# Kernel optimization log

Measured on AMD Instinct MI355X. Metric: run time of the kernel, lower is better.

Reference implementation:

```python
import jax, jax.numpy as jnp
import numpy as np

B, S, D = 4, 2048, 1024
D_K, D_V = 1024, 1024


def setup_inputs() -> dict:
    key = jax.random.key(0)
    ks = jax.random.split(key, 9)
    s = 1.0 / np.sqrt(D)
    return {
        "q_in": jax.random.normal(ks[0], (B, S, D), jnp.float32),
        "k_in": jax.random.normal(ks[1], (B, S, D), jnp.float32),
        "v_in": jax.random.normal(ks[2], (B, S, D), jnp.float32),
        "Wq": jax.random.normal(ks[3], (D, D_K), jnp.float32) * s,
        "bq": jnp.zeros((D_K,), jnp.float32),
        "Wk": jax.random.normal(ks[4], (D, D_K), jnp.float32) * s,
        "bk": jnp.zeros((D_K,), jnp.float32),
        "Wv": jax.random.normal(ks[5], (D, D_V), jnp.float32) * s,
        "bv": jnp.zeros((D_V,), jnp.float32),
    }


def reference(q_in, k_in, v_in, Wq, bq, Wk, bk, Wv, bv):
    q = jnp.einsum("bsd,dk->bsk", q_in, Wq) + bq  # [B,S,d_k]
    k = jnp.einsum("bsd,dk->bsk", k_in, Wk) + bk  # [B,S,d_k]
    v = jnp.einsum("bsd,dv->bsv", v_in, Wv) + bv  # [B,S,d_v]
    scores = jnp.einsum("bqk,bsk->bqs", q, k) / jnp.sqrt(jnp.float32(D_K))
    attn = jax.nn.softmax(scores, axis=-1)  # [B,S,S]
    return jnp.einsum("bqs,bsv->bqv", attn, v)
```

## Files before the change

kernel.cpp:

```cpp
#include <hip/hip_runtime.h>
#include <stdint.h>

#define B_  4
#define S_  2048
#define D_  1024
#define DK_ 1024
#define DV_ 1024

typedef __attribute__((ext_vector_type(8)))  short short8;
typedef __attribute__((ext_vector_type(16))) float floatx16;

#define ASYNC16(gsrc, ldst)                                                        \
  __builtin_amdgcn_global_load_lds(                                                \
      (const __attribute__((address_space(1))) unsigned int*)(gsrc),               \
      (__attribute__((address_space(3))) unsigned int*)(ldst), 16, 0, 0)

__device__ __forceinline__ unsigned short f2bf(float f) {
  union { float f; uint32_t u; } v; v.f = f;
  uint32_t r = v.u + 0x7fffu + ((v.u >> 16) & 1u);
  return (unsigned short)(r >> 16);
}

__global__ __launch_bounds__(256) void cvt_f32_bf16(const float* __restrict__ in,
                                                    unsigned short* __restrict__ out, int n4) {
  int i = blockIdx.x * blockDim.x + threadIdx.x;
  if (i >= n4) return;
  float4 v = ((const float4*)in)[i];
  ushort4 o;
  o.x = f2bf(v.x); o.y = f2bf(v.y); o.z = f2bf(v.z); o.w = f2bf(v.w);
  ((ushort4*)out)[i] = o;
}

__global__ __launch_bounds__(256) void transpose_f32_bf16(const float* __restrict__ in,
                                                          unsigned short* __restrict__ out,
                                                          int rows, int cols) {
  __shared__ float tile[32][33];
  int bx = blockIdx.x * 32, by = blockIdx.y * 32;
  int tx = threadIdx.x & 31, ty = threadIdx.x >> 5;
  for (int r = ty; r < 32; r += 8)
    tile[r][tx] = in[(long)(by + r) * cols + bx + tx];
  __syncthreads();
  for (int r = ty; r < 32; r += 8)
    out[(long)(bx + r) * rows + by + tx] = f2bf(tile[tx][r]);
}

__global__ __launch_bounds__(256) void transpose_bf16_batched(const unsigned short* __restrict__ in,
                                                              unsigned short* __restrict__ out,
                                                              int rows, int cols) {
  in  += (long)blockIdx.z * rows * cols;
  out += (long)blockIdx.z * rows * cols;
  __shared__ unsigned short tile[32][33];
  int bx = blockIdx.x * 32, by = blockIdx.y * 32;
  int tx = threadIdx.x & 31, ty = threadIdx.x >> 5;
  for (int r = ty; r < 32; r += 8)
    tile[r][tx] = in[(long)(by + r) * cols + bx + tx];
  __syncthreads();
  for (int r = ty; r < 32; r += 8)
    out[(long)(bx + r) * rows + by + tx] = tile[tx][r];
}

__device__ __forceinline__ void storeC(float* p, float v)          { *p = v; }
__device__ __forceinline__ void storeC(unsigned short* p, float v) { *p = f2bf(v); }

template <typename OutT, int NOUT>
__global__ __launch_bounds__(256)
void gemm_bt32(const unsigned short* __restrict__ A0, const unsigned short* __restrict__ A1,
               const unsigned short* __restrict__ A2, const unsigned short* __restrict__ Bm,
               OutT* __restrict__ C0, OutT* __restrict__ C1, OutT* __restrict__ C2,
               const float* __restrict__ b0, const float* __restrict__ b1,
               const float* __restrict__ b2,
               int N, int K, long sA, long sB, long sC, float scale) {
  __shared__ __align__(16) unsigned short As[2][128 * 32];
  __shared__ __align__(16) unsigned short Bs[2][128 * 32];
  const int tid  = threadIdx.x;
  const int lane = tid & 63, wave = tid >> 6;
  const int wm = (wave >> 1) * 64, wn = (wave & 1) * 64;
  const int lm = lane & 31;
  const int hi = lane >> 5;
  const long zb = blockIdx.z;
  const int m0  = blockIdx.y * 128;
  const int n0g = blockIdx.x * 128;

  const unsigned short* A = A0;
  OutT* C = C0;
  const float* bias = b0;
  int n0 = n0g;
  if (NOUT == 3) {
    int sel = n0g >> 10;
    n0 = n0g & 1023;
    if (sel == 1)      { A = A1; C = C1; bias = b1; }
    else if (sel == 2) { A = A2; C = C2; bias = b2; }
  }
  A += zb * sA;
  const unsigned short* Bp = Bm + zb * sB;
  C += zb * sC;

  const int rr   = lane >> 2;
  const int ccol = (((lane & 3) ^ (rr & 3)) << 3);
  const unsigned short* agA = A  + (long)(m0  + 16 * wave + rr) * K + ccol;
  const unsigned short* agB = Bp + (long)(n0g + 16 * wave + rr) * K + ccol;
  const unsigned short* ag0 = agA;
  const unsigned short* ag1 = agA + 32;
  const unsigned short* ag2 = agA + 64 * (long)K;
  const unsigned short* ag3 = agA + 64 * (long)K + 32;
  const unsigned short* bg0 = agB;
  const unsigned short* bg1 = agB + 32;
  const unsigned short* bg2 = agB + 64 * (long)K;
  const unsigned short* bg3 = agB + 64 * (long)K + 32;
  unsigned short* al0 = &As[0][wave * 512];
  unsigned short* al1 = &As[1][wave * 512];
  unsigned short* al2 = &As[0][(wave + 4) * 512];
  unsigned short* al3 = &As[1][(wave + 4) * 512];
  unsigned short* bl0 = &Bs[0][wave * 512];
  unsigned short* bl1 = &Bs[1][wave * 512];
  unsigned short* bl2 = &Bs[0][(wave + 4) * 512];
  unsigned short* bl3 = &Bs[1][(wave + 4) * 512];

  floatx16 acc[2][2] = {};

  for (int kt = 0; kt < K; kt += 64) {
    __syncthreads();
    ASYNC16(ag0, al0); ASYNC16(ag1, al1); ASYNC16(ag2, al2); ASYNC16(ag3, al3);
    ASYNC16(bg0, bl0); ASYNC16(bg1, bl1); ASYNC16(bg2, bl2); ASYNC16(bg3, bl3);
    __syncthreads();

#pragma unroll
    for (int s = 0; s < 4; s++) {
      const int h = s >> 1, hs = s & 1;
      const int blk = (((hs << 1) | hi) ^ (lm & 3)) << 3;
      short8 af[2], bf[2];
#pragma unroll
      for (int i = 0; i < 2; i++)
        af[i] = *(const short8*)&As[h][(wm + i * 32 + lm) * 32 + blk];
#pragma unroll
      for (int j = 0; j < 2; j++)
        bf[j] = *(const short8*)&Bs[h][(wn + j * 32 + lm) * 32 + blk];
#pragma unroll
      for (int i = 0; i < 2; i++)
#pragma unroll
        for (int j = 0; j < 2; j++)
          acc[i][j] = __builtin_amdgcn_mfma_f32_32x32x16_bf16(af[i], bf[j], acc[i][j], 0, 0, 0);
    }
    ag0 += 64; ag1 += 64; ag2 += 64; ag3 += 64;
    bg0 += 64; bg1 += 64; bg2 += 64; bg3 += 64;
  }

#pragma unroll
  for (int i = 0; i < 2; i++) {
#pragma unroll
    for (int j = 0; j < 2; j++) {
      const int col = n0 + wn + j * 32 + lm;
      const float bv = bias ? bias[col] : 0.f;
#pragma unroll
      for (int r = 0; r < 16; r++) {
        const int row = m0 + wm + i * 32 + (r & 3) + ((r >> 2) << 3) + (hi << 2);
        storeC(C + (long)row * N + col, acc[i][j][r] * scale + bv);
      }
    }
  }
}

__global__ __launch_bounds__(256) void softmax_rows(const float* __restrict__ Sc,
                                                    unsigned short* __restrict__ P) {
  const long row = blockIdx.x;
  const float* x = Sc + row * 2048;
  unsigned short* p = P + row * 2048;
  const int tid = threadIdx.x;
  float v[8];
  float m = -3.4e38f;
#pragma unroll
  for (int j = 0; j < 8; j++) { v[j] = x[tid + j * 256]; m = fmaxf(m, v[j]); }
#pragma unroll
  for (int off = 32; off > 0; off >>= 1) m = fmaxf(m, __shfl_xor(m, off, 64));
  __shared__ float redm[4], reds[4];
  if ((tid & 63) == 0) redm[tid >> 6] = m;
  __syncthreads();
  m = fmaxf(fmaxf(redm[0], redm[1]), fmaxf(redm[2], redm[3]));
  float s = 0.f;
#pragma unroll
  for (int j = 0; j < 8; j++) { v[j] = __expf(v[j] - m); s += v[j]; }
#pragma unroll
  for (int off = 32; off > 0; off >>= 1) s += __shfl_xor(s, off, 64);
  if ((tid & 63) == 0) reds[tid >> 6] = s;
  __syncthreads();
  s = reds[0] + reds[1] + reds[2] + reds[3];
  float inv = 1.f / s;
#pragma unroll
  for (int j = 0; j < 8; j++) p[tid + j * 256] = f2bf(v[j] * inv);
}

extern "C" void kernel_launch(void* const* d_in, const int* in_sizes, int n_in,
                              void* d_out, int out_size, void* d_ws, size_t ws_size,
                              hipStream_t stream) {
  const float* q_in = (const float*)d_in[0];
  const float* k_in = (const float*)d_in[1];
  const float* v_in = (const float*)d_in[2];
  const float* Wq   = (const float*)d_in[3];
  const float* bq   = (const float*)d_in[4];
  const float* Wk   = (const float*)d_in[5];
  const float* bk   = (const float*)d_in[6];
  const float* Wv   = (const float*)d_in[7];
  const float* bv   = (const float*)d_in[8];
  float* out = (float*)d_out;

  char* ws = (char*)d_ws;
  const long nX = (long)B_ * S_ * D_;
  const long nW = (long)D_ * DK_;
  unsigned short* qb  = (unsigned short*)(ws);
  unsigned short* kb  = qb + nX;
  unsigned short* vb  = kb + nX;
  unsigned short* WqT = vb + nX;
  unsigned short* WkT = WqT + nW;
  unsigned short* WvT = WkT + nW;
  unsigned short* Vb  = WvT + nW;
  unsigned short* Qb  = Vb + nX;
  unsigned short* Kb  = Qb + nX;
  unsigned short* Vt  = Kb + nX;
  float*          scores = (float*)ws;
  unsigned short* attn   = Vt + nX;

  dim3 blk(256);

  {
    int n4 = (int)(nX / 4);
    dim3 g(n4 / 256);
    cvt_f32_bf16<<<g, blk, 0, stream>>>(q_in, qb, n4);
    cvt_f32_bf16<<<g, blk, 0, stream>>>(k_in, kb, n4);
    cvt_f32_bf16<<<g, blk, 0, stream>>>(v_in, vb, n4);
  }
  {
    dim3 g(DK_ / 32, D_ / 32);
    transpose_f32_bf16<<<g, blk, 0, stream>>>(Wq, WqT, D_, DK_);
    transpose_f32_bf16<<<g, blk, 0, stream>>>(Wk, WkT, D_, DK_);
    transpose_f32_bf16<<<g, blk, 0, stream>>>(Wv, WvT, D_, DK_);
  }
  {
    dim3 g(3 * DK_ / 128, (B_ * S_) / 128, 1);
    gemm_bt32<unsigned short, 3><<<g, blk, 0, stream>>>(
        qb, kb, vb, WqT, Qb, Kb, Vb, bq, bk, bv, DK_, D_, 0, 0, 0, 1.f);
  }
  {
    dim3 g(DV_ / 32, S_ / 32, B_);
    transpose_bf16_batched<<<g, blk, 0, stream>>>(Vb, Vt, S_, DV_);
  }
  {
    dim3 g(S_ / 128, S_ / 128, B_);
    gemm_bt32<float, 1><<<g, blk, 0, stream>>>(
        Qb, nullptr, nullptr, Kb, scores, nullptr, nullptr, nullptr, nullptr, nullptr,
        S_, DK_, (long)S_ * DK_, (long)S_ * DK_, (long)S_ * S_, 0.03125f);
  }
  {
    dim3 g(B_ * S_);
    softmax_rows<<<g, blk, 0, stream>>>(scores, attn);
  }
  {
    dim3 g(DV_ / 128, S_ / 128, B_);
    gemm_bt32<float, 1><<<g, blk, 0, stream>>>(
        attn, nullptr, nullptr, Vt, out, nullptr, nullptr, nullptr, nullptr, nullptr,
        DV_, S_, (long)S_ * S_, (long)DV_ * S_, (long)S_ * DV_, 1.f);
  }
}
```

Measured before the change: 383.2 us.

## Store scores in bf16, batch conversion launches, drop LDS swizzle in GEMM

Scores from the QK^T GEMM are now written as bf16 instead of fp32, and the softmax reads them with vectorized 16-byte loads and writes packed output. This halves the traffic of the largest intermediate, at the cost of rounding the scores to bf16 before exp. The three input conversions and the three weight transposes each become one launch that uses blockIdx.z, removing launch overhead. The XOR swizzle on the GEMM shared-memory layout is removed, which may bring back LDS bank conflicts. The softmax also now reads a contiguous 8-element chunk per thread; since max and sum are reductions over the whole row, this stays correct.

```diff
diff --git a/kernel.cpp b/kernel.cpp
--- a/kernel.cpp
+++ b/kernel.cpp
@@ -20,20 +20,32 @@
   uint32_t r = v.u + 0x7fffu + ((v.u >> 16) & 1u);
   return (unsigned short)(r >> 16);
 }
-
-__global__ __launch_bounds__(256) void cvt_f32_bf16(const float* __restrict__ in,
-                                                    unsigned short* __restrict__ out, int n4) {
-  int i = blockIdx.x * blockDim.x + threadIdx.x;
+__device__ __forceinline__ float bf2f(unsigned short h) {
+  union { float f; uint32_t u; } v; v.u = ((uint32_t)h) << 16;
+  return v.f;
+}
+
+__global__ __launch_bounds__(256) void cvt3_f32_bf16(const float* __restrict__ a,
+                                                     const float* __restrict__ b,
+                                                     const float* __restrict__ c,
+                                                     unsigned short* __restrict__ out, int n4) {
+  const float* in = (blockIdx.z == 0) ? a : (blockIdx.z == 1) ? b : c;
+  unsigned short* o = out + (long)blockIdx.z * n4 * 4;
+  int i = blockIdx.x * 256 + threadIdx.x;
   if (i >= n4) return;
   float4 v = ((const float4*)in)[i];
-  ushort4 o;
-  o.x = f2bf(v.x); o.y = f2bf(v.y); o.z = f2bf(v.z); o.w = f2bf(v.w);
-  ((ushort4*)out)[i] = o;
-}
-
-__global__ __launch_bounds__(256) void transpose_f32_bf16(const float* __restrict__ in,
-                                                          unsigned short* __restrict__ out,
-                                                          int rows, int cols) {
+  ushort4 u;
+  u.x = f2bf(v.x); u.y = f2bf(v.y); u.z = f2bf(v.z); u.w = f2bf(v.w);
+  ((ushort4*)o)[i] = u;
+}
+
+__global__ __launch_bounds__(256) void transpose3_f32_bf16(const float* __restrict__ W0,
+                                                           const float* __restrict__ W1,
+                                                           const float* __restrict__ W2,
+                                                           unsigned short* __restrict__ out,
+                                                           int rows, int cols) {
+  const float* in = (blockIdx.z == 0) ? W0 : (blockIdx.z == 1) ? W1 : W2;
+  unsigned short* o = out + (long)blockIdx.z * rows * cols;
   __shared__ float tile[32][33];
   int bx = blockIdx.x * 32, by = blockIdx.y * 32;
   int tx = threadIdx.x & 31, ty = threadIdx.x >> 5;
@@ -41,7 +53,7 @@
     tile[r][tx] = in[(long)(by + r) * cols + bx + tx];
   __syncthreads();
   for (int r = ty; r < 32; r += 8)
-    out[(long)(bx + r) * rows + by + tx] = f2bf(tile[tx][r]);
+    o[(long)(bx + r) * rows + by + tx] = f2bf(tile[tx][r]);
 }
 
 __global__ __launch_bounds__(256) void transpose_bf16_batched(const unsigned short* __restrict__ in,
@@ -95,10 +107,10 @@
   const unsigned short* Bp = Bm + zb * sB;
   C += zb * sC;
 
-  const int rr   = lane >> 2;
-  const int ccol = (((lane & 3) ^ (rr & 3)) << 3);
-  const unsigned short* agA = A  + (long)(m0  + 16 * wave + rr) * K + ccol;
-  const unsigned short* agB = Bp + (long)(n0g + 16 * wave + rr) * K + ccol;
+  const int rr = lane >> 2;
+  const int cc = (lane & 3) * 8;
+  const unsigned short* agA = A  + (long)(m0  + 16 * wave + rr) * K + cc;
+  const unsigned short* agB = Bp + (long)(n0g + 16 * wave + rr) * K + cc;
   const unsigned short* ag0 = agA;
   const unsigned short* ag1 = agA + 32;
   const unsigned short* ag2 = agA + 64 * (long)K;
@@ -126,15 +138,15 @@
 
 #pragma unroll
     for (int s = 0; s < 4; s++) {
-      const int h = s >> 1, hs = s & 1;
-      const int blk = (((hs << 1) | hi) ^ (lm & 3)) << 3;
+      const int h   = s >> 1;
+      const int off = (s & 1) * 16 + hi * 8;
       short8 af[2], bf[2];
 #pragma unroll
       for (int i = 0; i < 2; i++)
-        af[i] = *(const short8*)&As[h][(wm + i * 32 + lm) * 32 + blk];
+        af[i] = *(const short8*)&As[h][(wm + i * 32 + lm) * 32 + off];
 #pragma unroll
       for (int j = 0; j < 2; j++)
-        bf[j] = *(const short8*)&Bs[h][(wn + j * 32 + lm) * 32 + blk];
+        bf[j] = *(const short8*)&Bs[h][(wn + j * 32 + lm) * 32 + off];
 #pragma unroll
       for (int i = 0; i < 2; i++)
 #pragma unroll
@@ -160,16 +172,15 @@
   }
 }
 
-__global__ __launch_bounds__(256) void softmax_rows(const float* __restrict__ Sc,
-                                                    unsigned short* __restrict__ P) {
+__global__ __launch_bounds__(256) void softmax_rows_bf16(const unsigned short* __restrict__ Sc,
+                                                         unsigned short* __restrict__ P) {
   const long row = blockIdx.x;
-  const float* x = Sc + row * 2048;
-  unsigned short* p = P + row * 2048;
   const int tid = threadIdx.x;
+  short8 xv = ((const short8*)(Sc + row * 2048))[tid];
   float v[8];
   float m = -3.4e38f;
 #pragma unroll
-  for (int j = 0; j < 8; j++) { v[j] = x[tid + j * 256]; m = fmaxf(m, v[j]); }
+  for (int j = 0; j < 8; j++) { v[j] = bf2f((unsigned short)xv[j]); m = fmaxf(m, v[j]); }
 #pragma unroll
   for (int off = 32; off > 0; off >>= 1) m = fmaxf(m, __shfl_xor(m, off, 64));
   __shared__ float redm[4], reds[4];
@@ -185,8 +196,10 @@
   __syncthreads();
   s = reds[0] + reds[1] + reds[2] + reds[3];
   float inv = 1.f / s;
-#pragma unroll
-  for (int j = 0; j < 8; j++) p[tid + j * 256] = f2bf(v[j] * inv);
+  short8 ov;
+#pragma unroll
+  for (int j = 0; j < 8; j++) ov[j] = (short)f2bf(v[j] * inv);
+  ((short8*)(P + row * 2048))[tid] = ov;
 }
 
 extern "C" void kernel_launch(void* const* d_in, const int* in_sizes, int n_in,
@@ -210,29 +223,23 @@
   unsigned short* kb  = qb + nX;
   unsigned short* vb  = kb + nX;
   unsigned short* WqT = vb + nX;
-  unsigned short* WkT = WqT + nW;
-  unsigned short* WvT = WkT + nW;
-  unsigned short* Vb  = WvT + nW;
+  unsigned short* Vb  = WqT + 3 * nW;
   unsigned short* Qb  = Vb + nX;
   unsigned short* Kb  = Qb + nX;
   unsigned short* Vt  = Kb + nX;
-  float*          scores = (float*)ws;
-  unsigned short* attn   = Vt + nX;
+  unsigned short* scoresB = (unsigned short*)ws;
+  unsigned short* attn    = Vt + nX;
 
   dim3 blk(256);
 
   {
     int n4 = (int)(nX / 4);
-    dim3 g(n4 / 256);
-    cvt_f32_bf16<<<g, blk, 0, stream>>>(q_in, qb, n4);
-    cvt_f32_bf16<<<g, blk, 0, stream>>>(k_in, kb, n4);
-    cvt_f32_bf16<<<g, blk, 0, stream>>>(v_in, vb, n4);
-  }
-  {
-    dim3 g(DK_ / 32, D_ / 32);
-    transpose_f32_bf16<<<g, blk, 0, stream>>>(Wq, WqT, D_, DK_);
-    transpose_f32_bf16<<<g, blk, 0, stream>>>(Wk, WkT, D_, DK_);
-    transpose_f32_bf16<<<g, blk, 0, stream>>>(Wv, WvT, D_, DK_);
+    dim3 g(n4 / 256, 1, 3);
+    cvt3_f32_bf16<<<g, blk, 0, stream>>>(q_in, k_in, v_in, qb, n4);
+  }
+  {
+    dim3 g(DK_ / 32, D_ / 32, 3);
+    transpose3_f32_bf16<<<g, blk, 0, stream>>>(Wq, Wk, Wv, WqT, D_, DK_);
   }
   {
     dim3 g(3 * DK_ / 128, (B_ * S_) / 128, 1);
@@ -245,13 +252,13 @@
   }
   {
     dim3 g(S_ / 128, S_ / 128, B_);
-    gemm_bt32<float, 1><<<g, blk, 0, stream>>>(
-        Qb, nullptr, nullptr, Kb, scores, nullptr, nullptr, nullptr, nullptr, nullptr,
+    gemm_bt32<unsigned short, 1><<<g, blk, 0, stream>>>(
+        Qb, nullptr, nullptr, Kb, scoresB, nullptr, nullptr, nullptr, nullptr, nullptr,
         S_, DK_, (long)S_ * DK_, (long)S_ * DK_, (long)S_ * S_, 0.03125f);
   }
   {
     dim3 g(B_ * S_);
-    softmax_rows<<<g, blk, 0, stream>>>(scores, attn);
+    softmax_rows_bf16<<<g, blk, 0, stream>>>(scoresB, attn);
   }
   {
     dim3 g(DV_ / 128, S_ / 128, B_);
```

After: 363.0 us. -5.3%, faster.
